# Kernel tuning notes

Hardware: AMD Instinct MI355X
Metric: run time of the kernel (lower is better)

Reference implementation:

```python
import jax, jax.numpy as jnp
import numpy as np
import math

B, L, DM, H, ALPHA = 8, 2048, 512, 8, 3
DH = DM // H
SK = min(ALPHA * math.ceil(math.log(L)), L)    # sample_k = U_part = 24
NTOP = min(ALPHA * math.ceil(math.log(L)), L)  # n_top u = 24


def _ln(x, w, b, eps=1e-8):
    # TF-style layernorm (eps inside sqrt), matching custom LayerNorm
    u = x.mean(-1, keepdims=True)
    s = ((x - u) ** 2).mean(-1, keepdims=True)
    return w * (x - u) / jnp.sqrt(s + eps) + b


def setup_inputs() -> dict:
    key = jax.random.key(0)
    ks = jax.random.split(key, 12)
    p = lambda k, shape: jax.random.normal(k, shape, dtype=jnp.float32) * 0.02
    return {
        'queries': jax.random.normal(ks[0], (B, L, DM), dtype=jnp.float32),
        'keys': jax.random.normal(ks[1], (B, L, DM), dtype=jnp.float32),
        'values': jax.random.normal(ks[2], (B, L, DM), dtype=jnp.float32),
        'padding_mask': jnp.ones((B, L), dtype=jnp.float32),
        'Wq': p(ks[3], (DM, DM)), 'bq': jnp.zeros((DM,), jnp.float32),
        'Wk': p(ks[4], (DM, DM)), 'bk': jnp.zeros((DM,), jnp.float32),
        'Wv': p(ks[5], (DM, DM)), 'bv': jnp.zeros((DM,), jnp.float32),
        'Wf': p(ks[6], (DM, DM)), 'bf': jnp.zeros((DM,), jnp.float32),
        'qln_w': jnp.ones((DM,), jnp.float32), 'qln_b': jnp.zeros((DM,), jnp.float32),
        'fln_w': jnp.ones((DM,), jnp.float32), 'fln_b': jnp.zeros((DM,), jnp.float32),
        'index_sample': jax.random.randint(ks[7], (L, SK), 0, L, dtype=jnp.int32),
    }


def reference(queries, keys, values, padding_mask, Wq, bq, Wk, bk, Wv, bv, Wf, bf,
              qln_w, qln_b, fln_w, fln_b, index_sample):
    Bq, Lq, Dm = queries.shape
    Lk = keys.shape[1]
    Dh = Dm // H
    # projections + head split -> (B, H, L, Dh)
    q = (_ln(queries, qln_w, qln_b) @ Wq + bq).reshape(Bq, Lq, H, Dh).transpose(0, 2, 1, 3)
    k = (keys @ Wk + bk).reshape(Bq, Lk, H, Dh).transpose(0, 2, 1, 3)
    v = (values @ Wv + bv).reshape(Bq, Lk, H, Dh).transpose(0, 2, 1, 3)
    # _prob_QK: random K sampling + sparsity measure + top-n_top query selection
    K_sample = k[:, :, index_sample, :]                        # (B,H,Lq,SK,Dh) irregular gather
    QKs = jnp.einsum('bhid,bhijd->bhij', q, K_sample)          # (B,H,Lq,SK)
    M = QKs.max(-1) - QKs.sum(-1) / Lk
    _, m_top = jax.lax.top_k(M, NTOP)                          # (B,H,u)
    q_red = jnp.take_along_axis(q, m_top[..., None], axis=2)   # (B,H,u,Dh)
    # NOTE: source scales by 1/sqrt(full hidden dim D), not head size
    scores = jnp.einsum('bhud,bhkd->bhuk', q_red, k) * (1.0 / math.sqrt(Dm))
    # ProbMask: causal (key <= selected query pos) AND padding at selected queries
    causal = jnp.arange(Lk)[None, None, None, :] <= m_top[..., None]   # (B,H,u,Lk)
    pad_ind = padding_mask[jnp.arange(Bq)[:, None, None], m_top]       # (B,H,u)
    mask = causal & (pad_ind[..., None] != 0)
    scores = jnp.where(mask, scores, -100000.0)
    # initial values = causal cumulative mean of V (with_mask branch)
    v_avg = jnp.cumsum(v, axis=2) / (jnp.cumsum(padding_mask, -1)[:, None, :, None] + 1e-12)
    attn = jax.nn.softmax(scores, axis=-1)
    upd = jnp.einsum('bhuk,bhkd->bhud', attn, v)               # sparse attention output
    bi = jnp.arange(Bq)[:, None, None]
    hi = jnp.arange(H)[None, :, None]
    out = v_avg.at[bi, hi, m_top].set(upd)                     # scatter selected rows back
    out = out.transpose(0, 2, 1, 3).reshape(Bq, Lq, Dm)
    out = out @ Wf + bf
    return _ln(out, fln_w, fln_b)
```

## Files before the change

kernel.cpp:

```cpp
#include <hip/hip_runtime.h>
#include <math.h>

#define L 2048
#define DM 512
#define B_ 8
#define H_ 8
#define DH 64
#define SK 24
#define NTOP 24
#define CHUNK 128
#define NCH (L / CHUNK)
#define VC 32
#define VR 64
#define ABUF 4096

typedef __attribute__((ext_vector_type(8))) short short8;
typedef __attribute__((ext_vector_type(8))) __bf16 bf16x8;
typedef __attribute__((ext_vector_type(4))) float f32x4;

__device__ inline unsigned short f2bf(float x) {
    unsigned u = __float_as_uint(x);
    unsigned r = (u + 0x7FFFu + ((u >> 16) & 1u)) >> 16;
    return (unsigned short)r;
}
__device__ inline float bf2f(unsigned short h) {
    return __uint_as_float(((unsigned)h) << 16);
}

__device__ inline f32x4 MFMA_BF16(short8 a, short8 b, f32x4 c) {
    return __builtin_amdgcn_mfma_f32_16x16x32_bf16(
        __builtin_bit_cast(bf16x8, a), __builtin_bit_cast(bf16x8, b), c, 0, 0, 0);
}

__device__ __forceinline__ void gload16(const unsigned short* g, unsigned short* l) {
    __builtin_amdgcn_global_load_lds(
        (const __attribute__((address_space(1))) void*)g,
        (__attribute__((address_space(3))) void*)l, 16, 0, 0);
}

template<bool WANTL>
__device__ inline void cvt8(const float4& x, const float4& y, short8& h, short8& l) {
    float v0 = x.x, v1 = x.y, v2 = x.z, v3 = x.w;
    float v4 = y.x, v5 = y.y, v6 = y.z, v7 = y.w;
    unsigned short h0 = f2bf(v0), h1 = f2bf(v1), h2 = f2bf(v2), h3 = f2bf(v3);
    unsigned short h4 = f2bf(v4), h5 = f2bf(v5), h6 = f2bf(v6), h7 = f2bf(v7);
    h[0] = (short)h0; h[1] = (short)h1; h[2] = (short)h2; h[3] = (short)h3;
    h[4] = (short)h4; h[5] = (short)h5; h[6] = (short)h6; h[7] = (short)h7;
    if (WANTL) {
        l[0] = (short)f2bf(v0 - bf2f(h0)); l[1] = (short)f2bf(v1 - bf2f(h1));
        l[2] = (short)f2bf(v2 - bf2f(h2)); l[3] = (short)f2bf(v3 - bf2f(h3));
        l[4] = (short)f2bf(v4 - bf2f(h4)); l[5] = (short)f2bf(v5 - bf2f(h5));
        l[6] = (short)f2bf(v6 - bf2f(h6)); l[7] = (short)f2bf(v7 - bf2f(h7));
    }
}

__device__ inline int lds_addr(int row, int kblk) {
    return row * 32 + ((kblk ^ ((row >> 1) & 3)) << 3);
}

__device__ inline float waveReduceSum(float v) {
    for (int o = 32; o > 0; o >>= 1) v += __shfl_down(v, o, 64);
    return v;
}

__global__ __launch_bounds__(256)
void prep_kernel(const float* __restrict__ queries,
                 const float* __restrict__ qlnw, const float* __restrict__ qlnb,
                 unsigned short* __restrict__ lnq_h, unsigned short* __restrict__ lnq_l,
                 const float* __restrict__ Wq, const float* __restrict__ Wk,
                 const float* __restrict__ Wv, const float* __restrict__ Wf,
                 unsigned short* __restrict__ wts,
                 const float* __restrict__ pad, float* __restrict__ denom) {
    __shared__ float shmem[32 * 33];
    int bid = blockIdx.x;
    int tid = threadIdx.x;
    if (bid < 16384) {
        int row = bid;
        const float* xr = queries + (size_t)row * DM;
        float2 v = *(const float2*)(xr + tid * 2);
        float s = v.x + v.y;
        float sq = v.x * v.x + v.y * v.y;
        float* red = shmem;
        float wsu = waveReduceSum(s);
        float wq = waveReduceSum(sq);
        int wid = tid >> 6, lane = tid & 63;
        if (lane == 0) { red[wid] = wsu; red[4 + wid] = wq; }
        __syncthreads();
        float tot = red[0] + red[1] + red[2] + red[3];
        float totq = red[4] + red[5] + red[6] + red[7];
        float mean = tot * (1.0f / DM);
        float var = totq * (1.0f / DM) - mean * mean;
        float inv = rsqrtf(var + 1e-8f);
        float w0 = qlnw[tid * 2], w1 = qlnw[tid * 2 + 1];
        float b0 = qlnb[tid * 2], b1 = qlnb[tid * 2 + 1];
        float o0 = w0 * (v.x - mean) * inv + b0;
        float o1 = w1 * (v.y - mean) * inv + b1;
        ushort2 hh, ll;
        hh.x = f2bf(o0); ll.x = f2bf(o0 - bf2f(hh.x));
        hh.y = f2bf(o1); ll.y = f2bf(o1 - bf2f(hh.y));
        *(ushort2*)(lnq_h + (size_t)row * DM + tid * 2) = hh;
        *(ushort2*)(lnq_l + (size_t)row * DM + tid * 2) = ll;
    } else if (bid < 16384 + 1024) {
        int idx = bid - 16384;
        int w = idx >> 8;
        int t256 = idx & 255;
        int n0 = (t256 & 15) * 32, k0 = (t256 >> 4) * 32;
        const float* W = (w == 0) ? Wq : (w == 1) ? Wk : (w == 2) ? Wv : Wf;
        unsigned short* th = wts + (size_t)w * 2 * 262144;
        unsigned short* tl = th + 262144;
        float (*ts)[33] = (float(*)[33])shmem;
        int r = tid >> 3, c = (tid & 7) * 4;
        float4 v = *(const float4*)(W + (size_t)(k0 + r) * 512 + n0 + c);
        ts[r][c] = v.x; ts[r][c + 1] = v.y; ts[r][c + 2] = v.z; ts[r][c + 3] = v.w;
        __syncthreads();
        float a0 = ts[c + 0][r], a1 = ts[c + 1][r], a2 = ts[c + 2][r], a3 = ts[c + 3][r];
        ushort4 h, l;
        h.x = f2bf(a0); l.x = f2bf(a0 - bf2f(h.x));
        h.y = f2bf(a1); l.y = f2bf(a1 - bf2f(h.y));
        h.z = f2bf(a2); l.z = f2bf(a2 - bf2f(h.z));
        h.w = f2bf(a3); l.w = f2bf(a3 - bf2f(h.w));
        *(ushort4*)(th + (size_t)(n0 + r) * 512 + k0 + c) = h;
        *(ushort4*)(tl + (size_t)(n0 + r) * 512 + k0 + c) = l;
    } else {
        int b = bid - (16384 + 1024);
        float* tot = shmem;
        const float* p = pad + (size_t)b * L;
        float loc[8];
        float s = 0.f;
#pragma unroll
        for (int u = 0; u < 8; u++) { s += p[tid * 8 + u]; loc[u] = s; }
        tot[tid] = s;
        __syncthreads();
        for (int off = 1; off < 256; off <<= 1) {
            float add = (tid >= off) ? tot[tid - off] : 0.f;
            __syncthreads();
            tot[tid] += add;
            __syncthreads();
        }
        float excl = tot[tid] - s;
#pragma unroll
        for (int u = 0; u < 8; u++) denom[(size_t)b * L + tid * 8 + u] = excl + loc[u];
    }
}

template<int TERMS, int OMODE, int ACVT>
__device__ __forceinline__
void gemm_body(unsigned short* smem,
               const unsigned short* __restrict__ Ah, const unsigned short* __restrict__ Al,
               const float* __restrict__ Af,
               const unsigned short* __restrict__ Bh, const unsigned short* __restrict__ Bl,
               const float* __restrict__ bias, float* __restrict__ C,
               unsigned short* __restrict__ Ch, int orig) {
    unsigned short* sAh = smem;
    unsigned short* sAl = smem + ABUF;
    unsigned short* sBh = smem + (TERMS == 3 ? 2 : 1) * ABUF;
    unsigned short* sBl = sBh + ABUF;

    int j = (orig & 7) * 64 + (orig >> 3);
    int n0 = (j & 3) * 128, m0 = (j >> 2) * 128;

    int tid = threadIdx.x;
    int lane = tid & 63, wv = tid >> 6;
    int wr = wv >> 1, wc = wv & 1;
    int lrow = lane & 15, g = lane >> 4;

    int f0 = tid, f1 = tid + 256;
    int row0 = f0 >> 2, k0b = f0 & 3;
    int row1 = f1 >> 2, k1b = f1 & 3;
    int sa0 = lds_addr(row0, k0b), sa1 = lds_addr(row1, k1b);
    int c0 = k0b * 8, c1 = k1b * 8;

    f32x4 acc[4][4];
#pragma unroll
    for (int mf = 0; mf < 4; mf++)
#pragma unroll
        for (int nf = 0; nf < 4; nf++) acc[mf][nf] = (f32x4){0.f, 0.f, 0.f, 0.f};

    short8 rAh0, rAh1, rAl0, rAl1, rBh0, rBh1, rBl0, rBl1;
    float4 fA00, fA01, fA10, fA11;

    auto LOAD = [&](int kt) {
        int k0 = kt * 32;
        if (ACVT) {
            fA00 = *(const float4*)(Af + (size_t)(m0 + row0) * 512 + k0 + c0);
            fA01 = *(const float4*)(Af + (size_t)(m0 + row0) * 512 + k0 + c0 + 4);
            fA10 = *(const float4*)(Af + (size_t)(m0 + row1) * 512 + k0 + c1);
            fA11 = *(const float4*)(Af + (size_t)(m0 + row1) * 512 + k0 + c1 + 4);
        } else {
            rAh0 = *(const short8*)(Ah + (size_t)(m0 + row0) * 512 + k0 + c0);
            rAh1 = *(const short8*)(Ah + (size_t)(m0 + row1) * 512 + k0 + c1);
            if (TERMS == 3) {
                rAl0 = *(const short8*)(Al + (size_t)(m0 + row0) * 512 + k0 + c0);
                rAl1 = *(const short8*)(Al + (size_t)(m0 + row1) * 512 + k0 + c1);
            }
        }
        rBh0 = *(const short8*)(Bh + (size_t)(n0 + row0) * 512 + k0 + c0);
        rBh1 = *(const short8*)(Bh + (size_t)(n0 + row1) * 512 + k0 + c1);
        if (TERMS >= 2) {
            rBl0 = *(const short8*)(Bl + (size_t)(n0 + row0) * 512 + k0 + c0);
            rBl1 = *(const short8*)(Bl + (size_t)(n0 + row1) * 512 + k0 + c1);
        }
    };
    auto STORE = [&]() {
        if (ACVT) {
            cvt8<TERMS == 3>(fA00, fA01, rAh0, rAl0);
            cvt8<TERMS == 3>(fA10, fA11, rAh1, rAl1);
        }
        *(short8*)&sAh[sa0] = rAh0;
        *(short8*)&sAh[sa1] = rAh1;
        if (TERMS == 3) {
            *(short8*)&sAl[sa0] = rAl0;
            *(short8*)&sAl[sa1] = rAl1;
        }
        *(short8*)&sBh[sa0] = rBh0;
        *(short8*)&sBh[sa1] = rBh1;
        if (TERMS >= 2) {
            *(short8*)&sBl[sa0] = rBl0;
            *(short8*)&sBl[sa1] = rBl1;
        }
    };

    int ra = wr * 64 + lrow;
    int rb = wc * 64 + lrow;
    int abase = ra * 32 + ((g ^ ((ra >> 1) & 3)) << 3);
    int bbase = rb * 32 + ((g ^ ((rb >> 1) & 3)) << 3);

    LOAD(0);
    for (int kt = 0; kt < 16; kt++) {
        STORE();
        __syncthreads();
        if (kt < 15) LOAD(kt + 1);
        short8 ah[4], al[4], bh[4], bl[4];
#pragma unroll
        for (int mf = 0; mf < 4; mf++) {
            ah[mf] = *(const short8*)&sAh[abase + mf * 512];
            if (TERMS == 3) al[mf] = *(const short8*)&sAl[abase + mf * 512];
        }
#pragma unroll
        for (int nf = 0; nf < 4; nf++) {
            bh[nf] = *(const short8*)&sBh[bbase + nf * 512];
            if (TERMS >= 2) bl[nf] = *(const short8*)&sBl[bbase + nf * 512];
        }
#pragma unroll
        for (int mf = 0; mf < 4; mf++)
#pragma unroll
            for (int nf = 0; nf < 4; nf++) {
                acc[mf][nf] = MFMA_BF16(ah[mf], bh[nf], acc[mf][nf]);
                if (TERMS >= 2) acc[mf][nf] = MFMA_BF16(ah[mf], bl[nf], acc[mf][nf]);
                if (TERMS == 3) acc[mf][nf] = MFMA_BF16(al[mf], bh[nf], acc[mf][nf]);
            }
        __syncthreads();
    }

    int crow0 = m0 + wr * 64 + (lane >> 4) * 4;
    int ccol0 = n0 + wc * 64 + lrow;
    float bb[4];
#pragma unroll
    for (int nf = 0; nf < 4; nf++) bb[nf] = bias[ccol0 + nf * 16];
#pragma unroll
    for (int mf = 0; mf < 4; mf++)
#pragma unroll
        for (int nf = 0; nf < 4; nf++)
#pragma unroll
            for (int r = 0; r < 4; r++) {
                float val = acc[mf][nf][r] + bb[nf];
                size_t idx = (size_t)(crow0 + mf * 16 + r) * 512 + ccol0 + nf * 16;
                if (OMODE != 2) C[idx] = val;
                if (OMODE != 0) Ch[idx] = f2bf(val);
            }
}

template<int TERMS, int OMODE>
__device__ __forceinline__
void gemm_body_gload(unsigned short* smem,
                     const unsigned short* __restrict__ Ah, const unsigned short* __restrict__ Al,
                     const unsigned short* __restrict__ Bh, const unsigned short* __restrict__ Bl,
                     const float* __restrict__ bias, float* __restrict__ C,
                     unsigned short* __restrict__ Ch, int orig) {
    unsigned short* sAh = smem;
    unsigned short* sAl = smem + ABUF;
    unsigned short* sBh = smem + (TERMS == 3 ? 2 : 1) * ABUF;
    unsigned short* sBl = sBh + ABUF;

    int j = (orig & 7) * 64 + (orig >> 3);
    int n0 = (j & 3) * 128, m0 = (j >> 2) * 128;

    int tid = threadIdx.x;
    int lane = tid & 63, wv = tid >> 6;
    int wr = wv >> 1, wc = wv & 1;
    int lrow = lane & 15, g = lane >> 4;

    int r0 = wv * 16 + (lane >> 2);
    int r1 = r0 + 64;
    int kpos = lane & 3;
    int s0col = (kpos ^ ((r0 >> 1) & 3)) * 8;
    int s1col = (kpos ^ ((r1 >> 1) & 3)) * 8;

    f32x4 acc[4][4];
#pragma unroll
    for (int mf = 0; mf < 4; mf++)
#pragma unroll
        for (int nf = 0; nf < 4; nf++) acc[mf][nf] = (f32x4){0.f, 0.f, 0.f, 0.f};

    auto GLOAD_ALL = [&](int kt) {
        int k0 = kt * 32;
        gload16(Ah + (size_t)(m0 + r0) * 512 + k0 + s0col, sAh + wv * 512);
        gload16(Ah + (size_t)(m0 + r1) * 512 + k0 + s1col, sAh + 2048 + wv * 512);
        if (TERMS == 3) {
            gload16(Al + (size_t)(m0 + r0) * 512 + k0 + s0col, sAl + wv * 512);
            gload16(Al + (size_t)(m0 + r1) * 512 + k0 + s1col, sAl + 2048 + wv * 512);
        }
        gload16(Bh + (size_t)(n0 + r0) * 512 + k0 + s0col, sBh + wv * 512);
        gload16(Bh + (size_t)(n0 + r1) * 512 + k0 + s1col, sBh + 2048 + wv * 512);
        if (TERMS >= 2) {
            gload16(Bl + (size_t)(n0 + r0) * 512 + k0 + s0col, sBl + wv * 512);
            gload16(Bl + (size_t)(n0 + r1) * 512 + k0 + s1col, sBl + 2048 + wv * 512);
        }
    };

    int ra = wr * 64 + lrow;
    int rb = wc * 64 + lrow;
    int abase = ra * 32 + ((g ^ ((ra >> 1) & 3)) << 3);
    int bbase = rb * 32 + ((g ^ ((rb >> 1) & 3)) << 3);

    for (int kt = 0; kt < 16; kt++) {
        GLOAD_ALL(kt);
        __syncthreads();
        short8 ah[4], al[4], bh[4], bl[4];
#pragma unroll
        for (int mf = 0; mf < 4; mf++) {
            ah[mf] = *(const short8*)&sAh[abase + mf * 512];
            if (TERMS == 3) al[mf] = *(const short8*)&sAl[abase + mf * 512];
        }
#pragma unroll
        for (int nf = 0; nf < 4; nf++) {
            bh[nf] = *(const short8*)&sBh[bbase + nf * 512];
            if (TERMS >= 2) bl[nf] = *(const short8*)&sBl[bbase + nf * 512];
        }
#pragma unroll
        for (int mf = 0; mf < 4; mf++)
#pragma unroll
            for (int nf = 0; nf < 4; nf++) {
                acc[mf][nf] = MFMA_BF16(ah[mf], bh[nf], acc[mf][nf]);
                if (TERMS >= 2) acc[mf][nf] = MFMA_BF16(ah[mf], bl[nf], acc[mf][nf]);
                if (TERMS == 3) acc[mf][nf] = MFMA_BF16(al[mf], bh[nf], acc[mf][nf]);
            }
        __syncthreads();
    }

    int crow0 = m0 + wr * 64 + (lane >> 4) * 4;
    int ccol0 = n0 + wc * 64 + lrow;
    float bb[4];
#pragma unroll
    for (int nf = 0; nf < 4; nf++) bb[nf] = bias[ccol0 + nf * 16];
#pragma unroll
    for (int mf = 0; mf < 4; mf++)
#pragma unroll
        for (int nf = 0; nf < 4; nf++)
#pragma unroll
            for (int r = 0; r < 4; r++) {
                float val = acc[mf][nf][r] + bb[nf];
                size_t idx = (size_t)(crow0 + mf * 16 + r) * 512 + ccol0 + nf * 16;
                if (OMODE != 2) C[idx] = val;
                if (OMODE != 0) Ch[idx] = f2bf(val);
            }
}

__global__ __launch_bounds__(256, 2)
void qkv_gemm(const unsigned short* __restrict__ lnq_h, const unsigned short* __restrict__ lnq_l,
              const float* __restrict__ keys, const float* __restrict__ values,
              const unsigned short* __restrict__ wq_h, const unsigned short* __restrict__ wq_l,
              const unsigned short* __restrict__ wk_h, const unsigned short* __restrict__ wk_l,
              const unsigned short* __restrict__ wv_h, const unsigned short* __restrict__ wv_l,
              const float* __restrict__ bq, const float* __restrict__ bk, const float* __restrict__ bv,
              float* __restrict__ qb, float* __restrict__ kb,
              unsigned short* __restrict__ kb_h, unsigned short* __restrict__ vb_h) {
    __shared__ __align__(16) unsigned short smem[4 * ABUF];
    int orig = blockIdx.x + 4 * blockIdx.y;
    if (blockIdx.z == 0)
        gemm_body_gload<3, 0>(smem, lnq_h, lnq_l, wq_h, wq_l, bq, qb, nullptr, orig);
    else if (blockIdx.z == 1)
        gemm_body<3, 1, 1>(smem, nullptr, nullptr, keys, wk_h, wk_l, bk, kb, kb_h, orig);
    else
        gemm_body<1, 2, 1>(smem, nullptr, nullptr, values, wv_h, wv_l, bv, nullptr, vb_h, orig);
}

__global__ __launch_bounds__(256, 2)
void fgemm_kernel(const unsigned short* __restrict__ Ah,
                  const unsigned short* __restrict__ Bh,
                  const float* __restrict__ bias, float* __restrict__ C) {
    __shared__ __align__(16) unsigned short smem[2 * ABUF];
    int orig = blockIdx.x + 4 * blockIdx.y;
    gemm_body_gload<1, 0>(smem, Ah, nullptr, Bh, nullptr, bias, C, nullptr, orig);
}

__global__ __launch_bounds__(256)
void sm_vsum_kernel(const float* __restrict__ q, const float* __restrict__ k,
                    const int* __restrict__ idx, float* __restrict__ M,
                    const unsigned short* __restrict__ vh, float* __restrict__ csum) {
    int bid = blockIdx.x;
    if (bid < 4096) {
        int b = bid & 7;
        int ig = bid >> 3;
        int wv = threadIdx.x >> 6, lane = threadIdx.x & 63;
        int i = ig * 4 + wv;
        const float* qrow = q + ((size_t)b * L + i) * DM + lane * 8;
        float4 q0 = *(const float4*)qrow;
        float4 q1 = *(const float4*)(qrow + 4);
        int myidx = 0;
        if (lane < SK) myidx = idx[i * SK + lane];
        float sj[SK];
#pragma unroll
        for (int j = 0; j < SK; j++) {
            int row = __shfl(myidx, j, 64);
            const float* kp = k + ((size_t)b * L + row) * DM + lane * 8;
            float4 k0 = *(const float4*)kp;
            float4 k1 = *(const float4*)(kp + 4);
            sj[j] = q0.x * k0.x + q0.y * k0.y + q0.z * k0.z + q0.w * k0.w
                  + q1.x * k1.x + q1.y * k1.y + q1.z * k1.z + q1.w * k1.w;
        }
        float mx = -1e30f, sm = 0.f;
#pragma unroll
        for (int j = 0; j < SK; j++) {
            float s = sj[j];
            s += __shfl_xor(s, 1, 64);
            s += __shfl_xor(s, 2, 64);
            s += __shfl_xor(s, 4, 64);
            mx = fmaxf(mx, s);
            sm += s;
        }
        if ((lane & 7) == 0) {
            int h = lane >> 3;
            M[((size_t)b * H_ + h) * L + i] = mx - sm * (1.0f / L);
        }
    } else {
        int t = bid - 4096;
        int c = t & (VC - 1), b = t >> 5;
        int d2 = threadIdx.x;
        size_t base = ((size_t)b * L + c * VR) * DM + d2 * 2;
        float a0 = 0.f, a1 = 0.f;
        for (int tt = 0; tt < VR; tt++) {
            unsigned v = *(const unsigned*)(vh + base + (size_t)tt * DM);
            a0 += bf2f((unsigned short)(v & 0xffff));
            a1 += bf2f((unsigned short)(v >> 16));
        }
        float2 st = {a0, a1};
        *(float2*)(csum + ((size_t)b * VC + c) * DM + d2 * 2) = st;
    }
}

__global__ __launch_bounds__(256)
void topk_vavg_kernel(const float* __restrict__ M, int* __restrict__ mtop,
                      const float* __restrict__ qb, const float* __restrict__ pad,
                      unsigned short* __restrict__ qsel, int* __restrict__ lim_arr,
                      const unsigned short* __restrict__ vh, const float* __restrict__ csum,
                      const float* __restrict__ denom, unsigned short* __restrict__ out_h) {
    int bid = blockIdx.x;
    if (bid < 64) {
        int bh = bid;
        int b = bh >> 3, h = bh & 7;
        int wv = threadIdx.x >> 6, lane = threadIdx.x & 63;
        __shared__ int sel_s[NTOP];
        if (wv == 0) {
            const float* Mr = M + (size_t)bh * L;
            float m[32];
#pragma unroll
            for (int r = 0; r < 32; r++) m[r] = Mr[r * 64 + lane];
            for (int it = 0; it < NTOP; it++) {
                float bv = -1e30f; int br = 0;
#pragma unroll
                for (int r = 0; r < 32; r++) {
                    bool better = m[r] > bv;
                    br = better ? r : br;
                    bv = better ? m[r] : bv;
                }
                int bt = (br << 6) | lane;
#pragma unroll
                for (int o = 1; o < 64; o <<= 1) {
                    float ov = __shfl_xor(bv, o, 64);
                    int ot = __shfl_xor(bt, o, 64);
                    bool take = (ov > bv) || (ov == bv && ot < bt);
                    bv = take ? ov : bv;
                    bt = take ? ot : bt;
                }
                if (lane == 0) { mtop[bh * NTOP + it] = bt; sel_s[it] = bt; }
                int rwin = bt >> 6;
                bool mine = (bt & 63) == lane;
#pragma unroll
                for (int r = 0; r < 32; r++)
                    if (mine && (r == rwin)) m[r] = -1e30f;
            }
        }
        __syncthreads();
        for (int u = wv; u < 32; u += 4) {
            if (u < NTOP) {
                int iq = sel_s[u];
                bool ok = pad[(size_t)b * L + iq] != 0.f;
                float sc = ok ? 0.044194173824159216f : 0.f;
                float qv = qb[((size_t)b * L + iq) * DM + h * DH + lane];
                qsel[((size_t)bh * 32 + u) * 64 + lane] = f2bf(qv * sc);
                if (lane == 0) lim_arr[bh * 32 + u] = ok ? iq : (L - 1);
            } else {
                qsel[((size_t)bh * 32 + u) * 64 + lane] = 0;
                if (lane == 0) lim_arr[bh * 32 + u] = -1;
            }
        }
    } else {
        int t = bid - 64;
        int c = t & (VC - 1), b = t >> 5;
        int d2 = threadIdx.x;
        float a0 = 0.f, a1 = 0.f;
        for (int cc = 0; cc < c; cc++) {
            float2 tt = *(const float2*)(csum + ((size_t)b * VC + cc) * DM + d2 * 2);
            a0 += tt.x; a1 += tt.y;
        }
        size_t base = ((size_t)b * L + c * VR) * DM + d2 * 2;
        for (int tt = 0; tt < VR; tt++) {
            unsigned v = *(const unsigned*)(vh + base + (size_t)tt * DM);
            a0 += bf2f((unsigned short)(v & 0xffff));
            a1 += bf2f((unsigned short)(v >> 16));
            float dn = denom[(size_t)b * L + c * VR + tt] + 1e-12f;
            unsigned o = (unsigned)f2bf(a0 / dn) | ((unsigned)f2bf(a1 / dn) << 16);
            *(unsigned*)(out_h + base + (size_t)tt * DM) = o;
        }
    }
}

__global__ __launch_bounds__(256)
void attn_chunk_mfma(const unsigned short* __restrict__ kbh,
                     const unsigned short* __restrict__ vbh,
                     const unsigned short* __restrict__ qsel,
                     const int* __restrict__ lim_arr,
                     float* __restrict__ part_m, float* __restrict__ part_s,
                     float* __restrict__ part_acc) {
    int c = blockIdx.x, bh = blockIdx.y;
    int b = bh >> 3, h = bh & 7;
    int j0 = c * CHUNK;
    __shared__ __align__(16) unsigned short KV[128 * 64];
    __shared__ __align__(16) unsigned short Ps[32 * 128];
    __shared__ __align__(16) unsigned short Qs[32 * 64];
    __shared__ float redm[4][32];
    __shared__ float reds[4][32];
    __shared__ int lims[32];

    int tid = threadIdx.x;
    int wv = tid >> 6, lane = tid & 63;
    int l15 = lane & 15, g = lane >> 4;

    const unsigned short* kpanel = kbh + ((size_t)b * L + j0) * DM + h * DH;
    short8 kreg[4];
#pragma unroll
    for (int l = 0; l < 4; l++) {
        int f = tid + l * 256;
        int jr = f >> 3, blk = f & 7;
        kreg[l] = *(const short8*)(kpanel + (size_t)jr * DM + blk * 8);
    }
    {
        int u = tid >> 3, blk = tid & 7;
        short8 qreg = *(const short8*)(qsel + ((size_t)bh * 32 + u) * 64 + blk * 8);
        *(short8*)&Qs[u * 64 + (((blk ^ (u & 7))) << 3)] = qreg;
    }
#pragma unroll
    for (int l = 0; l < 4; l++) {
        int f = tid + l * 256;
        int jr = f >> 3, blk = f & 7;
        *(short8*)&KV[jr * 64 + ((blk ^ (jr & 7)) << 3)] = kreg[l];
    }
    if (tid < 32) lims[tid] = lim_arr[bh * 32 + tid];
    __syncthreads();

    f32x4 sf[2][2];
#pragma unroll
    for (int mf = 0; mf < 2; mf++)
#pragma unroll
        for (int nf = 0; nf < 2; nf++) sf[mf][nf] = (f32x4){0.f, 0.f, 0.f, 0.f};
#pragma unroll
    for (int ks = 0; ks < 2; ks++) {
        short8 aq[2], bk[2];
#pragma unroll
        for (int mf = 0; mf < 2; mf++) {
            int u = mf * 16 + l15;
            int blk = (ks * 4 + g) ^ (u & 7);
            aq[mf] = *(const short8*)&Qs[u * 64 + (blk << 3)];
        }
#pragma unroll
        for (int nf = 0; nf < 2; nf++) {
            int jr = wv * 32 + nf * 16 + l15;
            int blk = (ks * 4 + g) ^ (jr & 7);
            bk[nf] = *(const short8*)&KV[jr * 64 + (blk << 3)];
        }
#pragma unroll
        for (int mf = 0; mf < 2; mf++)
#pragma unroll
            for (int nf = 0; nf < 2; nf++)
                sf[mf][nf] = MFMA_BF16(aq[mf], bk[nf], sf[mf][nf]);
    }

    const unsigned short* vpanel = vbh + ((size_t)b * L + j0) * DM + h * DH;
    short8 vreg[4];
#pragma unroll
    for (int l = 0; l < 4; l++) {
        int f = tid + l * 256;
        int jr = f >> 3, blk = f & 7;
        vreg[l] = *(const short8*)(vpanel + (size_t)jr * DM + blk * 8);
    }

    float sv[2][2][4];
    float mx[2][4];
#pragma unroll
    for (int mf = 0; mf < 2; mf++)
#pragma unroll
        for (int r = 0; r < 4; r++) {
            int u = mf * 16 + g * 4 + r;
            int limv = lims[u];
            float m = -1e30f;
#pragma unroll
            for (int nf = 0; nf < 2; nf++) {
                int jg = j0 + wv * 32 + nf * 16 + l15;
                float s = (jg <= limv) ? sf[mf][nf][r] : -1e30f;
                sv[mf][nf][r] = s;
                m = fmaxf(m, s);
            }
            m = fmaxf(m, __shfl_xor(m, 1, 64));
            m = fmaxf(m, __shfl_xor(m, 2, 64));
            m = fmaxf(m, __shfl_xor(m, 4, 64));
            m = fmaxf(m, __shfl_xor(m, 8, 64));
            mx[mf][r] = m;
        }
    if (l15 == 0) {
#pragma unroll
        for (int mf = 0; mf < 2; mf++)
#pragma unroll
            for (int r = 0; r < 4; r++)
                redm[wv][mf * 16 + g * 4 + r] = mx[mf][r];
    }
    __syncthreads();

    float lmax[2][4], smv[2][4];
#pragma unroll
    for (int mf = 0; mf < 2; mf++)
#pragma unroll
        for (int r = 0; r < 4; r++) {
            int u = mf * 16 + g * 4 + r;
            float m = fmaxf(fmaxf(redm[0][u], redm[1][u]),
                            fmaxf(redm[2][u], redm[3][u]));
            lmax[mf][r] = m;
            bool any = m > -1e29f;
            float sm = 0.f;
#pragma unroll
            for (int nf = 0; nf < 2; nf++) {
                float e = any ? __expf(sv[mf][nf][r] - m) : 0.f;
                sm += e;
                int jr = wv * 32 + nf * 16 + l15;
                Ps[u * 128 + (((jr >> 3) ^ (u & 7)) << 3) + (jr & 7)] = f2bf(e);
            }
            sm += __shfl_xor(sm, 1, 64);
            sm += __shfl_xor(sm, 2, 64);
            sm += __shfl_xor(sm, 4, 64);
            sm += __shfl_xor(sm, 8, 64);
            smv[mf][r] = sm;
        }
    if (l15 == 0) {
#pragma unroll
        for (int mf = 0; mf < 2; mf++)
#pragma unroll
            for (int r = 0; r < 4; r++)
                reds[wv][mf * 16 + g * 4 + r] = smv[mf][r];
    }
#pragma unroll
    for (int l = 0; l < 4; l++) {
        int f = tid + l * 256;
        int jr = f >> 3, blk = f & 7;
        short8 w = vreg[l];
        if ((jr >> 3) & 1) w = __builtin_shufflevector(w, w, 4, 5, 6, 7, 0, 1, 2, 3);
        *(short8*)&KV[jr * 64 + ((blk ^ (jr & 7)) << 3)] = w;
    }
    __syncthreads();

    if (wv == 0 && l15 == 0) {
#pragma unroll
        for (int mf = 0; mf < 2; mf++)
#pragma unroll
            for (int r = 0; r < 4; r++) {
                int u = mf * 16 + g * 4 + r;
                if (u < NTOP) {
                    float ss = reds[0][u] + reds[1][u] + reds[2][u] + reds[3][u];
                    part_m[(bh * NTOP + u) * NCH + c] = lmax[mf][r];
                    part_s[(bh * NTOP + u) * NCH + c] = ss;
                }
            }
    }

    f32x4 of[2];
    of[0] = (f32x4){0.f, 0.f, 0.f, 0.f};
    of[1] = (f32x4){0.f, 0.f, 0.f, 0.f};
    int d = wv * 16 + l15;
#pragma unroll
    for (int ks = 0; ks < 4; ks++) {
        unsigned short va[8];
#pragma unroll
        for (int i = 0; i < 8; i++) {
            int jr = ks * 32 + g * 8 + i;
            int addr = jr * 64 + (((d >> 3) ^ (jr & 7)) << 3)
                     + ((d & 7) ^ (((jr >> 3) & 1) << 2));
            va[i] = KV[addr];
        }
        short8 av;
#pragma unroll
        for (int i = 0; i < 8; i++) av[i] = (short)va[i];
        short8 bp[2];
#pragma unroll
        for (int nf = 0; nf < 2; nf++) {
            int u = nf * 16 + l15;
            int blk = (ks * 4 + g) ^ (u & 7);
            bp[nf] = *(const short8*)&Ps[u * 128 + (blk << 3)];
        }
#pragma unroll
        for (int nf = 0; nf < 2; nf++)
            of[nf] = MFMA_BF16(av, bp[nf], of[nf]);
    }
#pragma unroll
    for (int nf = 0; nf < 2; nf++) {
        int u = nf * 16 + l15;
        if (u < NTOP) {
#pragma unroll
            for (int r = 0; r < 4; r++)
                part_acc[((size_t)(bh * NTOP + u) * NCH + c) * 64 + wv * 16 + g * 4 + r] =
                    of[nf][r];
        }
    }
}

__global__ __launch_bounds__(256)
void attn_merge_kernel(const float* __restrict__ part_m, const float* __restrict__ part_s,
                       const float* __restrict__ part_acc, const int* __restrict__ mtop,
                       unsigned short* __restrict__ pre_h) {
    int ug = blockIdx.x;
    int bh = blockIdx.y;
    int b = bh >> 3, h = bh & 7;
    int tid = threadIdx.x;
    int u = ug * 4 + (tid >> 6);
    int d = tid & 63;
    int base = (bh * NTOP + u) * NCH;
    float m = -1e30f;
#pragma unroll
    for (int c = 0; c < NCH; c++) m = fmaxf(m, part_m[base + c]);
    float s = 0.f, o = 0.f;
#pragma unroll
    for (int c = 0; c < NCH; c++) {
        float w = __expf(part_m[base + c] - m);
        s += part_s[base + c] * w;
        o = fmaf(part_acc[(size_t)(base + c) * 64 + d], w, o);
    }
    o /= s;
    int iq = mtop[bh * NTOP + u];
    pre_h[((size_t)b * L + iq) * DM + h * DH + d] = f2bf(o);
}

__global__ __launch_bounds__(256)
void ln_kernel(const float* __restrict__ x, const float* __restrict__ w,
               const float* __restrict__ bvec, float* __restrict__ out) {
    int row = blockIdx.x;
    const float* xr = x + (size_t)row * DM;
    float* orow = out + (size_t)row * DM;
    int tid = threadIdx.x;
    float2 v = *(const float2*)(xr + tid * 2);
    float s = v.x + v.y;
    float sq = v.x * v.x + v.y * v.y;
    __shared__ float red[8];
    float ws = waveReduceSum(s);
    float wq = waveReduceSum(sq);
    int wid = tid >> 6, lane = tid & 63;
    if (lane == 0) { red[wid] = ws; red[4 + wid] = wq; }
    __syncthreads();
    float tot = red[0] + red[1] + red[2] + red[3];
    float totq = red[4] + red[5] + red[6] + red[7];
    float mean = tot * (1.0f / DM);
    float var = totq * (1.0f / DM) - mean * mean;
    float inv = rsqrtf(var + 1e-8f);
    float w0 = w[tid * 2], w1 = w[tid * 2 + 1];
    float b0 = bvec[tid * 2], b1 = bvec[tid * 2 + 1];
    float2 o;
    o.x = w0 * (v.x - mean) * inv + b0;
    o.y = w1 * (v.y - mean) * inv + b1;
    *(float2*)(orow + tid * 2) = o;
}

extern "C" void kernel_launch(void* const* d_in, const int* in_sizes, int n_in,
                              void* d_out, int out_size, void* d_ws, size_t ws_size,
                              hipStream_t stream) {
    const float* queries = (const float*)d_in[0];
    const float* keys    = (const float*)d_in[1];
    const float* values  = (const float*)d_in[2];
    const float* pad     = (const float*)d_in[3];
    const float* Wq = (const float*)d_in[4];  const float* bq = (const float*)d_in[5];
    const float* Wk = (const float*)d_in[6];  const float* bk = (const float*)d_in[7];
    const float* Wv = (const float*)d_in[8];  const float* bv = (const float*)d_in[9];
    const float* Wf = (const float*)d_in[10]; const float* bfv = (const float*)d_in[11];
    const float* qlnw = (const float*)d_in[12]; const float* qlnb = (const float*)d_in[13];
    const float* flnw = (const float*)d_in[14]; const float* flnb = (const float*)d_in[15];
    const int* idx = (const int*)d_in[16];

    float* ws = (float*)d_ws;
    const size_t NE = (size_t)B_ * L * DM;
    float* qb    = ws;
    float* kb    = ws + NE;
    unsigned short* vb_h = (unsigned short*)(ws + 2 * NE);
    unsigned short* kb_h = vb_h + NE;
    unsigned short* qsel = (unsigned short*)(ws + 3 * NE);
    int* lim_arr = (int*)(qsel + 64 * 32 * 64);
    float* Mbuf  = ws + 4 * NE;
    float* denom = Mbuf + (size_t)B_ * H_ * L;
    float* csum  = denom + (size_t)B_ * L;
    int*   mtop  = (int*)(csum + (size_t)B_ * VC * DM);
    unsigned short* bfr = (unsigned short*)(mtop + 2048);
    unsigned short* pre_h = bfr;
    unsigned short* wts   = bfr + NE;
    unsigned short* wq_h = wts;              unsigned short* wq_l = wts + 262144;
    unsigned short* wk_h = wts + 2 * 262144; unsigned short* wk_l = wts + 3 * 262144;
    unsigned short* wv_h = wts + 4 * 262144; unsigned short* wv_l = wts + 5 * 262144;
    unsigned short* wf_h = wts + 6 * 262144; unsigned short* wf_l = wts + 7 * 262144;

    float* tmp = (float*)d_out;
    unsigned short* lnq_h = (unsigned short*)d_out;
    unsigned short* lnq_l = lnq_h + NE;
    float* part_m   = tmp;
    float* part_s   = part_m + 64 * NTOP * NCH;
    float* part_acc = part_s + 64 * NTOP * NCH;

    prep_kernel<<<16384 + 1024 + 8, 256, 0, stream>>>(
        queries, qlnw, qlnb, lnq_h, lnq_l, Wq, Wk, Wv, Wf, wts, pad, denom);

    dim3 gq(4, 128, 3);
    qkv_gemm<<<gq, 256, 0, stream>>>(lnq_h, lnq_l, keys, values,
                                     wq_h, wq_l, wk_h, wk_l, wv_h, wv_l,
                                     bq, bk, bv, qb, kb, kb_h, vb_h);

    sm_vsum_kernel<<<4096 + 256, 256, 0, stream>>>(qb, kb, idx, Mbuf, vb_h, csum);
    topk_vavg_kernel<<<64 + 256, 256, 0, stream>>>(Mbuf, mtop, qb, pad, qsel, lim_arr,
                                                   vb_h, csum, denom, pre_h);
    dim3 gc(NCH, 64);
    attn_chunk_mfma<<<gc, 256, 0, stream>>>(kb_h, vb_h, qsel, lim_arr,
                                            part_m, part_s, part_acc);
    dim3 gmg(6, 64);
    attn_merge_kernel<<<gmg, 256, 0, stream>>>(part_m, part_s, part_acc, mtop, pre_h);
    dim3 gg(4, 128);
    fgemm_kernel<<<gg, 256, 0, stream>>>(pre_h, wf_h, bfv, (float*)d_out);
    ln_kernel<<<B_ * L, 256, 0, stream>>>((float*)d_out, flnw, flnb, (float*)d_out);
}
```

Before: 222.0 us.

## Double-buffer LDS tiles in global-load GEMM to overlap loads with MFMA

Turns the direct-to-LDS GEMM body into a two-stage pipeline: the next k-tile is issued into the alternate LDS buffer before computing on the current one. A partial vmcnt wait replaces the full sync, so memory latency can hide behind MFMA work. Shared memory doubles for the Q projection branch of qkv_gemm and for fgemm, which raises LDS pressure. The hand-written waitcnt counts must match the number of loads issued per stage to stay correct.

```diff
diff --git a/kernel.cpp b/kernel.cpp
--- a/kernel.cpp
+++ b/kernel.cpp
@@ -272,15 +272,13 @@
 
 template<int TERMS, int OMODE>
 __device__ __forceinline__
-void gemm_body_gload(unsigned short* smem,
-                     const unsigned short* __restrict__ Ah, const unsigned short* __restrict__ Al,
-                     const unsigned short* __restrict__ Bh, const unsigned short* __restrict__ Bl,
-                     const float* __restrict__ bias, float* __restrict__ C,
-                     unsigned short* __restrict__ Ch, int orig) {
-    unsigned short* sAh = smem;
-    unsigned short* sAl = smem + ABUF;
-    unsigned short* sBh = smem + (TERMS == 3 ? 2 : 1) * ABUF;
-    unsigned short* sBl = sBh + ABUF;
+void gemm_body_gload_db(unsigned short* smem,
+                        const unsigned short* __restrict__ Ah, const unsigned short* __restrict__ Al,
+                        const unsigned short* __restrict__ Bh, const unsigned short* __restrict__ Bl,
+                        const float* __restrict__ bias, float* __restrict__ C,
+                        unsigned short* __restrict__ Ch, int orig) {
+    constexpr int ARR = (TERMS == 3) ? 4 : ((TERMS >= 2) ? 3 : 2);
+    constexpr int AOFF_B = (TERMS == 3) ? 2 : 1;
 
     int j = (orig & 7) * 64 + (orig >> 3);
     int n0 = (j & 3) * 128, m0 = (j >> 2) * 128;
@@ -302,19 +300,20 @@
 #pragma unroll
         for (int nf = 0; nf < 4; nf++) acc[mf][nf] = (f32x4){0.f, 0.f, 0.f, 0.f};
 
-    auto GLOAD_ALL = [&](int kt) {
+    auto GLOAD = [&](int kt, int buf) {
         int k0 = kt * 32;
-        gload16(Ah + (size_t)(m0 + r0) * 512 + k0 + s0col, sAh + wv * 512);
-        gload16(Ah + (size_t)(m0 + r1) * 512 + k0 + s1col, sAh + 2048 + wv * 512);
+        unsigned short* base = smem + buf * (ARR * ABUF);
+        gload16(Ah + (size_t)(m0 + r0) * 512 + k0 + s0col, base + wv * 512);
+        gload16(Ah + (size_t)(m0 + r1) * 512 + k0 + s1col, base + 2048 + wv * 512);
         if (TERMS == 3) {
-            gload16(Al + (size_t)(m0 + r0) * 512 + k0 + s0col, sAl + wv * 512);
-            gload16(Al + (size_t)(m0 + r1) * 512 + k0 + s1col, sAl + 2048 + wv * 512);
-        }
-        gload16(Bh + (size_t)(n0 + r0) * 512 + k0 + s0col, sBh + wv * 512);
-        gload16(Bh + (size_t)(n0 + r1) * 512 + k0 + s1col, sBh + 2048 + wv * 512);
+            gload16(Al + (size_t)(m0 + r0) * 512 + k0 + s0col, base + ABUF + wv * 512);
+            gload16(Al + (size_t)(m0 + r1) * 512 + k0 + s1col, base + ABUF + 2048 + wv * 512);
+        }
+        gload16(Bh + (size_t)(n0 + r0) * 512 + k0 + s0col, base + AOFF_B * ABUF + wv * 512);
+        gload16(Bh + (size_t)(n0 + r1) * 512 + k0 + s1col, base + AOFF_B * ABUF + 2048 + wv * 512);
         if (TERMS >= 2) {
-            gload16(Bl + (size_t)(n0 + r0) * 512 + k0 + s0col, sBl + wv * 512);
-            gload16(Bl + (size_t)(n0 + r1) * 512 + k0 + s1col, sBl + 2048 + wv * 512);
+            gload16(Bl + (size_t)(n0 + r0) * 512 + k0 + s0col, base + (AOFF_B + 1) * ABUF + wv * 512);
+            gload16(Bl + (size_t)(n0 + r1) * 512 + k0 + s1col, base + (AOFF_B + 1) * ABUF + 2048 + wv * 512);
         }
     };
 
@@ -323,9 +322,22 @@
     int abase = ra * 32 + ((g ^ ((ra >> 1) & 3)) << 3);
     int bbase = rb * 32 + ((g ^ ((rb >> 1) & 3)) << 3);
 
+    GLOAD(0, 0);
     for (int kt = 0; kt < 16; kt++) {
-        GLOAD_ALL(kt);
-        __syncthreads();
+        if (kt < 15) {
+            GLOAD(kt + 1, (kt + 1) & 1);
+            if constexpr (TERMS == 3) asm volatile("s_waitcnt vmcnt(8)" ::: "memory");
+            else                      asm volatile("s_waitcnt vmcnt(4)" ::: "memory");
+        } else {
+            asm volatile("s_waitcnt vmcnt(0)" ::: "memory");
+        }
+        __builtin_amdgcn_s_barrier();
+        __builtin_amdgcn_sched_barrier(0);
+        const unsigned short* base = smem + (kt & 1) * (ARR * ABUF);
+        const unsigned short* sAh = base;
+        const unsigned short* sAl = base + ABUF;
+        const unsigned short* sBh = base + AOFF_B * ABUF;
+        const unsigned short* sBl = base + (AOFF_B + 1) * ABUF;
         short8 ah[4], al[4], bh[4], bl[4];
 #pragma unroll
         for (int mf = 0; mf < 4; mf++) {
@@ -345,7 +357,8 @@
                 if (TERMS >= 2) acc[mf][nf] = MFMA_BF16(ah[mf], bl[nf], acc[mf][nf]);
                 if (TERMS == 3) acc[mf][nf] = MFMA_BF16(al[mf], bh[nf], acc[mf][nf]);
             }
-        __syncthreads();
+        __builtin_amdgcn_sched_barrier(0);
+        __builtin_amdgcn_s_barrier();
     }
 
     int crow0 = m0 + wr * 64 + (lane >> 4) * 4;
@@ -375,10 +388,10 @@
               const float* __restrict__ bq, const float* __restrict__ bk, const float* __restrict__ bv,
               float* __restrict__ qb, float* __restrict__ kb,
               unsigned short* __restrict__ kb_h, unsigned short* __restrict__ vb_h) {
-    __shared__ __align__(16) unsigned short smem[4 * ABUF];
+    __shared__ __align__(16) unsigned short smem[8 * ABUF];
     int orig = blockIdx.x + 4 * blockIdx.y;
     if (blockIdx.z == 0)
-        gemm_body_gload<3, 0>(smem, lnq_h, lnq_l, wq_h, wq_l, bq, qb, nullptr, orig);
+        gemm_body_gload_db<3, 0>(smem, lnq_h, lnq_l, wq_h, wq_l, bq, qb, nullptr, orig);
     else if (blockIdx.z == 1)
         gemm_body<3, 1, 1>(smem, nullptr, nullptr, keys, wk_h, wk_l, bk, kb, kb_h, orig);
     else
@@ -389,9 +402,9 @@
 void fgemm_kernel(const unsigned short* __restrict__ Ah,
                   const unsigned short* __restrict__ Bh,
                   const float* __restrict__ bias, float* __restrict__ C) {
-    __shared__ __align__(16) unsigned short smem[2 * ABUF];
+    __shared__ __align__(16) unsigned short smem[4 * ABUF];
     int orig = blockIdx.x + 4 * blockIdx.y;
-    gemm_body_gload<1, 0>(smem, Ah, nullptr, Bh, nullptr, bias, C, nullptr, orig);
+    gemm_body_gload_db<1, 0>(smem, Ah, nullptr, Bh, nullptr, bias, C, nullptr, orig);
 }
 
 __global__ __launch_bounds__(256)
```

Measured after the change: 225.4 us. About the same (+1.5%).
